# Performance work log

Measured on AMD Instinct MI355X. Metric: run time of the kernel, lower is better.

Reference implementation:

```python
import jax, jax.numpy as jnp
import numpy as np

NEG_SLOPE = 0.2

def symlog(v):
    return jnp.sign(v) * jnp.log1p(jnp.abs(v))

def conv1d(v, w, b):
    # v: (N, Cin, L), w: (Cout, Cin, 3), 'same' padding, stride 1
    out = jax.lax.conv_general_dilated(v, w, (1,), 'SAME',
                                       dimension_numbers=('NCH', 'OIH', 'NCH'))
    return out + b[None, :, None]

def glorot(key, shape, fan_in, fan_out):
    s = jnp.sqrt(6.0 / (fan_in + fan_out))
    return jax.random.uniform(key, shape, jnp.float32, -s, s)

def setup_inputs() -> dict:
    N, L, E = 20000, 128, 320000
    IN, H, C, OHC = 512, 8, 32, 8
    key = jax.random.key(0)
    ks = jax.random.split(key, 12)
    x = jax.random.normal(ks[0], (N, IN), jnp.float32)
    onehot = jax.random.uniform(ks[1], (N, L), jnp.float32)
    src = jax.random.randint(ks[2], (E,), 0, N)
    off = jax.random.randint(ks[3], (E,), 1, N)
    dst = (src + off) % N  # guarantees no self loops
    adj = jnp.stack([src, dst], axis=0).astype(jnp.int64)
    lin_w = glorot(ks[4], (IN + OHC, H * C), IN + OHC, H * C)
    att_l = glorot(ks[5], (1, H, C), C, C)
    att_r = glorot(ks[6], (1, H, C), C, C)
    bias = jnp.zeros((H * C,), jnp.float32)
    conv1_w = glorot(ks[7], (8, 1, 3), 3, 24)
    conv1_b = jnp.zeros((8,), jnp.float32)
    conv2_w = glorot(ks[8], (16, 8, 3), 24, 48)
    conv2_b = jnp.zeros((16,), jnp.float32)
    lin2_w = glorot(ks[9], (16, OHC), 16, OHC)
    lin2_b = jnp.zeros((OHC,), jnp.float32)
    return {"x": x, "onehot": onehot, "adj": adj, "n_nodes": N,
            "lin_w": lin_w, "att_l": att_l, "att_r": att_r, "bias": bias,
            "conv1_w": conv1_w, "conv1_b": conv1_b,
            "conv2_w": conv2_w, "conv2_b": conv2_b,
            "lin2_w": lin2_w, "lin2_b": lin2_b}

def reference(x, onehot, adj, n_nodes, lin_w, att_l, att_r, bias,
              conv1_w, conv1_b, conv2_w, conv2_b, lin2_w, lin2_b):
    N = n_nodes
    H, C = att_l.shape[1], att_l.shape[2]
    # one-hot conv pipe: sort -> symlog -> conv-relu x2 -> global avg pool -> linear
    prepared = symlog(jnp.sort(onehot, axis=-1))[:, None, :]  # (N,1,L)
    h = jax.nn.relu(conv1d(prepared, conv1_w, conv1_b))
    h = jax.nn.relu(conv1d(h, conv2_w, conv2_b))
    readout = h.mean(axis=-1) @ lin2_w + lin2_b  # (N, OHC)
    xin = jnp.concatenate([x, readout], axis=-1)
    xh = (xin @ lin_w).reshape(N, H, C)
    al = (xh * att_l).sum(axis=-1)  # (N,H) sending alphas
    ar = (xh * att_r).sum(axis=-1)  # (N,H) receiving alphas
    # add self loops (input adj has none, so remove_self_loops is a no-op)
    loops = jnp.arange(N, dtype=adj.dtype)
    src = jnp.concatenate([adj[0], loops])
    dst = jnp.concatenate([adj[1], loops])
    # GAT-style attention with segment softmax over receiving nodes
    alpha = jax.nn.leaky_relu(al[src] + ar[dst], NEG_SLOPE)  # (Etot,H)
    amax = jax.ops.segment_max(alpha, dst, num_segments=N)
    ex = jnp.exp(alpha - amax[dst])
    denom = jax.ops.segment_sum(ex, dst, num_segments=N)
    alpha = ex / denom[dst]
    # weight + scatter-add aggregate
    wx = xh[src] * alpha[..., None]  # (Etot,H,C)
    new_x = jax.ops.segment_sum(wx, dst, num_segments=N).reshape(N, H * C) + bias
    new_onehot = jax.ops.segment_sum(onehot[src], dst, num_segments=N) + onehot
    return new_x, new_onehot
```

## Files before the change

### kernel.cpp

```cpp
#include <hip/hip_runtime.h>

#define NEG_SLOPE 0.2f

typedef __attribute__((ext_vector_type(4))) float f32x4;
typedef __attribute__((ext_vector_type(2))) float f32x2;
typedef __attribute__((ext_vector_type(8))) short short8;

__device__ __forceinline__ f32x2 mk2(float a, float b) { f32x2 r; r[0] = a; r[1] = b; return r; }

__device__ __forceinline__ f32x2 FMA2(f32x2 a, f32x2 b, f32x2 c) {
#if __has_builtin(__builtin_elementwise_fma)
    return __builtin_elementwise_fma(a, b, c);
#else
    f32x2 r; r[0] = fmaf(a[0], b[0], c[0]); r[1] = fmaf(a[1], b[1], c[1]); return r;
#endif
}

__device__ __forceinline__ ushort f2bf(float f) {
    uint u = __float_as_uint(f);
    u += 0x7FFFu + ((u >> 16) & 1u);
    return (ushort)(u >> 16);
}
__device__ __forceinline__ float bflo(uint u) { return __uint_as_float(u << 16); }
__device__ __forceinline__ float bfhi(uint u) { return __uint_as_float(u & 0xffff0000u); }


__global__ __launch_bounds__(256) void k_conv_wave(
    const float* __restrict__ x, const float* __restrict__ onehot,
    const float* __restrict__ c1w, const float* __restrict__ c1b,
    const float* __restrict__ c2w, const float* __restrict__ c2b,
    const float* __restrict__ l2w, const float* __restrict__ l2b,
    ushort* __restrict__ xpadA, uint* __restrict__ ohb, int* __restrict__ cursor, int N) {
    __shared__ ushort Hall[4][1056];

    const int gid = blockIdx.x * 256 + threadIdx.x;
    if (gid < N) cursor[gid] = 0;

    const int wave = threadIdx.x >> 6;
    const int lane = threadIdx.x & 63;
    const int n = blockIdx.x * 4 + wave;
    if (n >= N) return;
    ushort* H = Hall[wave];

    const int nt = n >> 6, g16 = (n >> 4) & 3, r16 = n & 15;
    const size_t qstep = ((size_t)nt*17)*4 + g16;

    {
        const float* xp = &x[(size_t)n*512 + lane*8];
        float4 lo = *reinterpret_cast<const float4*>(xp);
        float4 hi = *reinterpret_cast<const float4*>(xp + 4);
        uint4 w;
        w.x = (uint)f2bf(lo.x) | ((uint)f2bf(lo.y) << 16);
        w.y = (uint)f2bf(lo.z) | ((uint)f2bf(lo.w) << 16);
        w.z = (uint)f2bf(hi.x) | ((uint)f2bf(hi.y) << 16);
        w.w = (uint)f2bf(hi.z) | ((uint)f2bf(hi.w) << 16);
        const size_t a = (qstep + (size_t)(lane >> 2)*4)*512 + ((lane & 3)*16 + r16)*8;
        *reinterpret_cast<uint4*>(&xpadA[a]) = w;
    }

    float2 in2 = *reinterpret_cast<const float2*>(&onehot[(size_t)n * 128 + lane * 2]);
    ohb[(size_t)n*64 + lane] = (uint)f2bf(in2.x) | ((uint)f2bf(in2.y) << 16);
    float v0 = log1pf(in2.x);
    float v1 = log1pf(in2.y);

    #pragma unroll
    for (int k = 2; k <= 128; k <<= 1) {
        const bool asc = ((lane & (k >> 1)) == 0);
        #pragma unroll
        for (int j = k >> 1; j >= 2; j >>= 1) {
            const int m = j >> 1;
            float p0 = __shfl_xor(v0, m, 64);
            float p1 = __shfl_xor(v1, m, 64);
            const bool keepmin = (((lane & m) == 0) == asc);
            v0 = keepmin ? fminf(v0, p0) : fmaxf(v0, p0);
            v1 = keepmin ? fminf(v1, p1) : fmaxf(v1, p1);
        }
        float lo = fminf(v0, v1), hi = fmaxf(v0, v1);
        v0 = asc ? lo : hi;
        v1 = asc ? hi : lo;
    }

    float pm = __shfl_up(v1, 1, 64); if (lane == 0)  pm = 0.f;
    float pp = __shfl_down(v0, 1, 64); if (lane == 63) pp = 0.f;

    float h0[8], h1[8];
    {
        const f32x2 xm = mk2(pm, v0), x0 = mk2(v0, v1), xp2 = mk2(v1, pp);
        #pragma unroll
        for (int c = 0; c < 8; ++c) {
            const float w0 = c1w[c*3+0], w1 = c1w[c*3+1], w2 = c1w[c*3+2], b = c1b[c];
            f32x2 h = FMA2(xm, mk2(w0, w0), FMA2(x0, mk2(w1, w1), FMA2(xp2, mk2(w2, w2), mk2(b, b))));
            h0[c] = fmaxf(h[0], 0.f);
            h1[c] = fmaxf(h[1], 0.f);
        }
    }

    {
        if (lane == 0) {
            const uint4 z = make_uint4(0,0,0,0);
            *reinterpret_cast<uint4*>(&H[0*8])   = z;
            *reinterpret_cast<uint4*>(&H[130*8]) = z;
            *reinterpret_cast<uint4*>(&H[65*8])  = z;
        }
        uint4 w0, w1;
        w0.x = (uint)f2bf(h0[0]) | ((uint)f2bf(h0[1]) << 16);
        w0.y = (uint)f2bf(h0[2]) | ((uint)f2bf(h0[3]) << 16);
        w0.z = (uint)f2bf(h0[4]) | ((uint)f2bf(h0[5]) << 16);
        w0.w = (uint)f2bf(h0[6]) | ((uint)f2bf(h0[7]) << 16);
        w1.x = (uint)f2bf(h1[0]) | ((uint)f2bf(h1[1]) << 16);
        w1.y = (uint)f2bf(h1[2]) | ((uint)f2bf(h1[3]) << 16);
        w1.z = (uint)f2bf(h1[4]) | ((uint)f2bf(h1[5]) << 16);
        w1.w = (uint)f2bf(h1[6]) | ((uint)f2bf(h1[7]) << 16);
        *reinterpret_cast<uint4*>(&H[(66 + lane)*8]) = w0;
        *reinterpret_cast<uint4*>(&H[(lane + 1)*8])  = w1;
    }

    const int co = lane & 15;
    const int g2 = lane >> 4;
    short8 bfrag;
    #pragma unroll
    for (int j = 0; j < 8; ++j) bfrag[j] = 0;
    if (g2 < 3) {
        #pragma unroll
        for (int j = 0; j < 8; ++j) bfrag[j] = (short)f2bf(c2w[(co*8 + j)*3 + g2]);
    }
    const float bias_c = c2b[co];
    const f32x4 zacc = (f32x4)0.f;

    float poolv = 0.f;
    #pragma unroll
    for (int s = 0; s < 8; ++s) {
        const int qq = s*16 + co + g2;
        const int slot = (qq >> 1) + (qq & 1)*66;
        short8 afrag = *reinterpret_cast<const short8*>(&H[slot*8]);
        f32x4 d = __builtin_amdgcn_mfma_f32_16x16x32_bf16(afrag, bfrag, zacc, 0, 0, 0);
        poolv += fmaxf(d[0] + bias_c, 0.f);
        poolv += fmaxf(d[1] + bias_c, 0.f);
        poolv += fmaxf(d[2] + bias_c, 0.f);
        poolv += fmaxf(d[3] + bias_c, 0.f);
    }
    poolv += __shfl_xor(poolv, 16, 64);
    poolv += __shfl_xor(poolv, 32, 64);

    float rout = (lane < 8) ? l2b[lane] : 0.f;
    #pragma unroll
    for (int c = 0; c < 16; ++c) {
        float pc = __shfl(poolv, c, 64);
        if (lane < 8) rout = fmaf(pc * (1.f/128.f), l2w[c*8 + lane], rout);
    }
    {
        const size_t qb = (qstep + 16u*4u)*512;
        if (lane < 4) {
            const int i0 = 2*lane, i1 = 2*lane + 1;
            float lo = __shfl(rout, i0, 64);
            float hi = __shfl(rout, i1, 64);
            uint w = (uint)f2bf(lo) | ((uint)f2bf(hi) << 16);
            *reinterpret_cast<uint*>(&xpadA[qb + r16*8 + lane*2]) = w;
        } else if (lane < 7) {
            const int kc = lane - 3;
            const uint4 z = make_uint4(0,0,0,0);
            *reinterpret_cast<uint4*>(&xpadA[qb + (kc*16 + r16)*8]) = z;
        }
    }
}

__global__ __launch_bounds__(256) void k_prep(
    const float* __restrict__ lin_w, ushort* __restrict__ BtT,
    const int* __restrict__ dst, int* __restrict__ cursor, int E) {
    const int gid = blockIdx.x * 256 + threadIdx.x;
    if (gid < E) atomicAdd(&cursor[dst[gid]], 1);
    const int col = blockIdx.x;
    if (col < 256) {
        const int cs = col >> 4, fcol = col & 15;
        for (int k = threadIdx.x; k < 544; k += 256) {
            float v = (k < 520) ? lin_w[(size_t)k*256 + col] : 0.f;
            const int s = k >> 5, kc = (k >> 3) & 3, j = k & 7;
            BtT[(size_t)(s*16 + cs)*512 + (kc*16 + fcol)*8 + j] = f2bf(v);
        }
    }
}

__global__ __launch_bounds__(1024) void k_scan(int* __restrict__ deg, int* __restrict__ row_start, int N) {
    __shared__ int wsum[16];
    const int t = threadIdx.x;
    const int w = t >> 6, ln = t & 63;
    const int base = t * 20;
    int v[20];
    int run = 0;
    #pragma unroll
    for (int i = 0; i < 20; ++i) {
        const int idx = base + i;
        int d = 0;
        if (idx < N) { d = deg[idx]; deg[idx] = 0; }
        run += d;
        v[i] = run;
    }
    int s = run;
    #pragma unroll
    for (int d = 1; d < 64; d <<= 1) {
        int u = __shfl_up(s, d, 64);
        if (ln >= d) s += u;
    }
    if (ln == 63) wsum[w] = s;
    __syncthreads();
    if (w == 0) {
        int ws = (ln < 16) ? wsum[ln] : 0;
        int e2 = ws;
        #pragma unroll
        for (int d = 1; d < 16; d <<= 1) {
            int u = __shfl_up(e2, d, 64);
            if (ln >= d) e2 += u;
        }
        if (ln < 16) wsum[ln] = e2 - ws;
    }
    __syncthreads();
    const int off = (s - run) + wsum[w];
    if (t == 0) row_start[0] = 0;
    #pragma unroll
    for (int i = 0; i < 20; ++i) {
        const int idx = base + i;
        if (idx < N) row_start[idx + 1] = off + v[i];
    }
}

__global__ __launch_bounds__(128) void k_gemm_mfma(
    const ushort* __restrict__ xpadA, const ushort* __restrict__ BtT,
    const float* __restrict__ att_l, const float* __restrict__ att_r,
    ushort* __restrict__ xhb, float* __restrict__ al, float* __restrict__ ar,
    const int* __restrict__ src, const int* __restrict__ dst,
    const int* __restrict__ row_start, int* __restrict__ cursor, int* __restrict__ csr,
    int N, int E) {
    __shared__ __align__(16) float ep[64*36];

    const int t = threadIdx.x;
    const int wv = t >> 6, lane = t & 63;

    const int nwg = gridDim.x;
    const int q = nwg >> 3, r = nwg & 7;
    const int xcd = blockIdx.x & 7, idx = blockIdx.x >> 3;
    const int logical = (xcd < r ? xcd*(q+1) : r*(q+1) + (xcd-r)*q) + idx;
    const int lt = logical >> 3;
    const int ch = logical & 7;
    const int m0 = lt * 64;
    const int c0 = ch * 32;
    const int cs = ch * 2;

    const ushort* A0 = xpadA + ((size_t)(lt*17)*4 + wv*2)*512 + lane*8;
    const ushort* A1 = A0 + 512;
    const ushort* B0 = BtT + (size_t)(cs + 0)*512 + lane*8;
    const ushort* B1 = BtT + (size_t)(cs + 1)*512 + lane*8;

    f32x4 acc00 = (f32x4)0.f, acc01 = (f32x4)0.f, acc10 = (f32x4)0.f, acc11 = (f32x4)0.f;

    short8 a0[4], a1[4], b0[4], b1[4];
#define LOADSET(B_, S_)                                                       \
    {                                                                         \
        a0[B_] = *reinterpret_cast<const short8*>(A0 + (size_t)(S_)*2048);    \
        a1[B_] = *reinterpret_cast<const short8*>(A1 + (size_t)(S_)*2048);    \
        b0[B_] = *reinterpret_cast<const short8*>(B0 + (size_t)(S_)*8192);    \
        b1[B_] = *reinterpret_cast<const short8*>(B1 + (size_t)(S_)*8192);    \
    }
    LOADSET(0, 0)
    LOADSET(1, 1)
    LOADSET(2, 2)
    #pragma unroll
    for (int s = 0; s < 17; ++s) {
        const int b = s & 3;
        if (s + 3 < 17) LOADSET((s + 3) & 3, s + 3)
        acc00 = __builtin_amdgcn_mfma_f32_16x16x32_bf16(a0[b], b0[b], acc00, 0, 0, 0);
        acc01 = __builtin_amdgcn_mfma_f32_16x16x32_bf16(a0[b], b1[b], acc01, 0, 0, 0);
        acc10 = __builtin_amdgcn_mfma_f32_16x16x32_bf16(a1[b], b0[b], acc10, 0, 0, 0);
        acc11 = __builtin_amdgcn_mfma_f32_16x16x32_bf16(a1[b], b1[b], acc11, 0, 0, 0);
    }
#undef LOADSET

    {
        const int e = blockIdx.x * 128 + t;
        if (e < E) {
            const int d = dst[e];
            const int p = atomicAdd(&cursor[d], 1);
            csr[row_start[d] + p] = src[e];
        }
    }

    {
        const int rq = (lane >> 4) * 4;
        const int cb = lane & 15;
        #pragma unroll
        for (int r2 = 0; r2 < 4; ++r2) {
            ep[(wv*32 +      rq + r2)*36 +      cb] = acc00[r2];
            ep[(wv*32 +      rq + r2)*36 + 16 + cb] = acc01[r2];
            ep[(wv*32 + 16 + rq + r2)*36 +      cb] = acc10[r2];
            ep[(wv*32 + 16 + rq + r2)*36 + 16 + cb] = acc11[r2];
        }
    }
    __syncthreads();
    {
        const int rl = t >> 1;
        const int half = t & 1;
        const int row = m0 + rl;
        if (row < N) {
            const float* sp = &ep[rl*36 + half*16];
            float vals[16];
            #pragma unroll
            for (int i = 0; i < 16; ++i) vals[i] = sp[i];
            uint u[8];
            #pragma unroll
            for (int i = 0; i < 8; ++i)
                u[i] = (uint)f2bf(vals[2*i]) | ((uint)f2bf(vals[2*i+1]) << 16);
            ushort* db = &xhb[(size_t)row*256 + c0 + half*16];
            *reinterpret_cast<uint4*>(db)     = make_uint4(u[0], u[1], u[2], u[3]);
            *reinterpret_cast<uint4*>(db + 8) = make_uint4(u[4], u[5], u[6], u[7]);
            float pl = 0.f, pr = 0.f;
            #pragma unroll
            for (int i = 0; i < 16; ++i) {
                pl = fmaf(vals[i], att_l[c0 + half*16 + i], pl);
                pr = fmaf(vals[i], att_r[c0 + half*16 + i], pr);
            }
            pl += __shfl_xor(pl, 1, 64);
            pr += __shfl_xor(pr, 1, 64);
            if (half == 0) {
                al[(size_t)row*8 + ch] = pl;
                ar[(size_t)row*8 + ch] = pr;
            }
        }
    }
}

__global__ __launch_bounds__(256) void k_agg(
    const ushort* __restrict__ xhb,
    const float* __restrict__ al, const float* __restrict__ ar,
    const float* __restrict__ onehot, const uint* __restrict__ ohb,
    const float* __restrict__ bias,
    const int* __restrict__ row_start, const int* __restrict__ csr,
    float* __restrict__ out_x, float* __restrict__ out_oh, int N) {
    const int wave = threadIdx.x >> 6;
    const int lane = threadIdx.x & 63;
    const int half = lane >> 5;
    const int ln = lane & 31;
    const int n = blockIdx.x * 8 + wave * 2 + half;
    if (n >= N) return;
    const int h = ln >> 2;
    const float ard = ar[(size_t)n*8 + h];

    float a_self = al[(size_t)n*8 + h] + ard;
    a_self = fmaxf(a_self, NEG_SLOPE * a_self);
    float e_self = __expf(a_self);
    uint4 xsb = *reinterpret_cast<const uint4*>(&xhb[(size_t)n*256 + ln*8]);
    float acc0 = e_self * bflo(xsb.x), acc1 = e_self * bfhi(xsb.x);
    float acc2 = e_self * bflo(xsb.y), acc3 = e_self * bfhi(xsb.y);
    float acc4 = e_self * bflo(xsb.z), acc5 = e_self * bfhi(xsb.z);
    float acc6 = e_self * bflo(xsb.w), acc7 = e_self * bfhi(xsb.w);
    float den = e_self;
    float oh0 = 0.f, oh1 = 0.f, oh2 = 0.f, oh3 = 0.f;

    const int beg = row_start[n], end = row_start[n+1];
    int i = beg;
    for (; i + 1 < end; i += 2) {
        const int s0 = csr[i], s1 = csr[i+1];
        const float al0 = al[(size_t)s0*8 + h], al1 = al[(size_t)s1*8 + h];
        const uint4 x0 = *reinterpret_cast<const uint4*>(&xhb[(size_t)s0*256 + ln*8]);
        const uint4 x1 = *reinterpret_cast<const uint4*>(&xhb[(size_t)s1*256 + ln*8]);
        const uint2 o0 = *reinterpret_cast<const uint2*>(&ohb[(size_t)s0*64 + ln*2]);
        const uint2 o1 = *reinterpret_cast<const uint2*>(&ohb[(size_t)s1*64 + ln*2]);
        float a0 = al0 + ard; a0 = fmaxf(a0, NEG_SLOPE * a0);
        float a1 = al1 + ard; a1 = fmaxf(a1, NEG_SLOPE * a1);
        const float e0 = __expf(a0), e1 = __expf(a1);
        acc0 = fmaf(e0, bflo(x0.x), fmaf(e1, bflo(x1.x), acc0));
        acc1 = fmaf(e0, bfhi(x0.x), fmaf(e1, bfhi(x1.x), acc1));
        acc2 = fmaf(e0, bflo(x0.y), fmaf(e1, bflo(x1.y), acc2));
        acc3 = fmaf(e0, bfhi(x0.y), fmaf(e1, bfhi(x1.y), acc3));
        acc4 = fmaf(e0, bflo(x0.z), fmaf(e1, bflo(x1.z), acc4));
        acc5 = fmaf(e0, bfhi(x0.z), fmaf(e1, bfhi(x1.z), acc5));
        acc6 = fmaf(e0, bflo(x0.w), fmaf(e1, bflo(x1.w), acc6));
        acc7 = fmaf(e0, bfhi(x0.w), fmaf(e1, bfhi(x1.w), acc7));
        den += e0 + e1;
        oh0 += bflo(o0.x) + bflo(o1.x);
        oh1 += bfhi(o0.x) + bfhi(o1.x);
        oh2 += bflo(o0.y) + bflo(o1.y);
        oh3 += bfhi(o0.y) + bfhi(o1.y);
    }
    if (i < end) {
        const int s0 = csr[i];
        float a0 = al[(size_t)s0*8 + h] + ard;
        a0 = fmaxf(a0, NEG_SLOPE * a0);
        const float e0 = __expf(a0);
        const uint4 x0 = *reinterpret_cast<const uint4*>(&xhb[(size_t)s0*256 + ln*8]);
        const uint2 o0 = *reinterpret_cast<const uint2*>(&ohb[(size_t)s0*64 + ln*2]);
        acc0 = fmaf(e0, bflo(x0.x), acc0);
        acc1 = fmaf(e0, bfhi(x0.x), acc1);
        acc2 = fmaf(e0, bflo(x0.y), acc2);
        acc3 = fmaf(e0, bfhi(x0.y), acc3);
        acc4 = fmaf(e0, bflo(x0.z), acc4);
        acc5 = fmaf(e0, bfhi(x0.z), acc5);
        acc6 = fmaf(e0, bflo(x0.w), acc6);
        acc7 = fmaf(e0, bfhi(x0.w), acc7);
        den += e0;
        oh0 += bflo(o0.x);
        oh1 += bfhi(o0.x);
        oh2 += bflo(o0.y);
        oh3 += bfhi(o0.y);
    }
    const float inv = 1.f / den;
    const float4 bv0 = *reinterpret_cast<const float4*>(&bias[ln*8]);
    const float4 bv1 = *reinterpret_cast<const float4*>(&bias[ln*8 + 4]);
    float4 q0, q1;
    q0.x = fmaf(acc0, inv, bv0.x); q0.y = fmaf(acc1, inv, bv0.y);
    q0.z = fmaf(acc2, inv, bv0.z); q0.w = fmaf(acc3, inv, bv0.w);
    q1.x = fmaf(acc4, inv, bv1.x); q1.y = fmaf(acc5, inv, bv1.y);
    q1.z = fmaf(acc6, inv, bv1.z); q1.w = fmaf(acc7, inv, bv1.w);
    *reinterpret_cast<float4*>(&out_x[(size_t)n*256 + ln*8])     = q0;
    *reinterpret_cast<float4*>(&out_x[(size_t)n*256 + ln*8 + 4]) = q1;
    const float4 so = *reinterpret_cast<const float4*>(&onehot[(size_t)n*128 + ln*4]);
    float4 oo;
    oo.x = oh0 + 2.f*so.x;
    oo.y = oh1 + 2.f*so.y;
    oo.z = oh2 + 2.f*so.z;
    oo.w = oh3 + 2.f*so.w;
    *reinterpret_cast<float4*>(&out_oh[(size_t)n*128 + ln*4]) = oo;
}

extern "C" void kernel_launch(void* const* d_in, const int* in_sizes, int n_in,
                              void* d_out, int out_size, void* d_ws, size_t ws_size,
                              hipStream_t stream) {
    const float* x      = (const float*)d_in[0];
    const float* onehot = (const float*)d_in[1];
    const int*   adj    = (const int*)d_in[2];
    const float* lin_w  = (const float*)d_in[4];
    const float* att_l  = (const float*)d_in[5];
    const float* att_r  = (const float*)d_in[6];
    const float* bias   = (const float*)d_in[7];
    const float* c1w    = (const float*)d_in[8];
    const float* c1b    = (const float*)d_in[9];
    const float* c2w    = (const float*)d_in[10];
    const float* c2b    = (const float*)d_in[11];
    const float* l2w    = (const float*)d_in[12];
    const float* l2b    = (const float*)d_in[13];

    const int N = in_sizes[0] / 512;
    const int E = in_sizes[2] / 2;
    const int* src = adj;
    const int* dst = adj + E;

    float* out_x  = (float*)d_out;
    float* out_oh = out_x + (size_t)N * 256;

    const int NT = (N + 63) / 64;

    ushort* xpadA    = (ushort*)d_ws;
    ushort* BtT      = xpadA + (size_t)NT * 17 * 2048;
    ushort* xhb      = BtT + (size_t)17 * 8192;
    uint*   ohb      = (uint*)(xhb + (size_t)N * 256);
    float*  al       = (float*)(ohb + (size_t)N * 64);
    float*  ar       = al + (size_t)N * 8;
    int*   row_start = (int*)(ar + (size_t)N * 8);
    int*   cursor    = row_start + (N + 1);
    int*   csr       = cursor + N;

    const int EB = (E + 255) / 256;
    const int GB = NT * 8;

    k_conv_wave<<<(N + 3) / 4, 256, 0, stream>>>(x, onehot, c1w, c1b, c2w, c2b, l2w, l2b, xpadA, ohb, cursor, N);
    k_prep<<<EB, 256, 0, stream>>>(lin_w, BtT, dst, cursor, E);
    k_scan<<<1, 1024, 0, stream>>>(cursor, row_start, N);
    k_gemm_mfma<<<GB, 128, 0, stream>>>(xpadA, BtT, att_l, att_r, xhb, al, ar,
                                        src, dst, row_start, cursor, csr, N, E);
    k_agg<<<(N + 7) / 8, 256, 0, stream>>>(xhb, al, ar, onehot, ohb, bias, row_start, csr, out_x, out_oh, N);
}
```

Measured before the change: 163.5 us.

## Halve GEMM row tile and fold degree counting into conv kernel

The MFMA GEMM now computes 32-row tiles, with one 16-row MFMA strip per wave instead of two. This doubles the number of workgroups and adds an occupancy hint in the launch bounds. The epilogue is reworked so four threads share each row, with an extra shuffle step for the attention dot products. Destination-degree counting moves from the prep kernel into the conv kernel, and the cursor array is zeroed with a memset beforehand. The lin_w reformatting becomes its own small 256-block kernel. The aim is better GPU fill and less time spent in the serial prep launch, at the cost of more redundant B-tile loads per output row.

```diff
diff --git a/kernel.cpp b/kernel.cpp
--- a/kernel.cpp
+++ b/kernel.cpp
@@ -30,11 +30,12 @@
     const float* __restrict__ c1w, const float* __restrict__ c1b,
     const float* __restrict__ c2w, const float* __restrict__ c2b,
     const float* __restrict__ l2w, const float* __restrict__ l2b,
-    ushort* __restrict__ xpadA, uint* __restrict__ ohb, int* __restrict__ cursor, int N) {
+    ushort* __restrict__ xpadA, uint* __restrict__ ohb,
+    const int* __restrict__ dstv, int* __restrict__ cursor, int N, int E) {
     __shared__ ushort Hall[4][1056];
 
     const int gid = blockIdx.x * 256 + threadIdx.x;
-    if (gid < N) cursor[gid] = 0;
+    if (gid < E) atomicAdd(&cursor[dstv[gid]], 1);
 
     const int wave = threadIdx.x >> 6;
     const int lane = threadIdx.x & 63;
@@ -164,19 +165,14 @@
     }
 }
 
-__global__ __launch_bounds__(256) void k_prep(
-    const float* __restrict__ lin_w, ushort* __restrict__ BtT,
-    const int* __restrict__ dst, int* __restrict__ cursor, int E) {
-    const int gid = blockIdx.x * 256 + threadIdx.x;
-    if (gid < E) atomicAdd(&cursor[dst[gid]], 1);
+__global__ __launch_bounds__(256) void k_prepB(
+    const float* __restrict__ lin_w, ushort* __restrict__ BtT) {
     const int col = blockIdx.x;
-    if (col < 256) {
-        const int cs = col >> 4, fcol = col & 15;
-        for (int k = threadIdx.x; k < 544; k += 256) {
-            float v = (k < 520) ? lin_w[(size_t)k*256 + col] : 0.f;
-            const int s = k >> 5, kc = (k >> 3) & 3, j = k & 7;
-            BtT[(size_t)(s*16 + cs)*512 + (kc*16 + fcol)*8 + j] = f2bf(v);
-        }
+    const int cs = col >> 4, fcol = col & 15;
+    for (int k = threadIdx.x; k < 544; k += 256) {
+        float v = (k < 520) ? lin_w[(size_t)k*256 + col] : 0.f;
+        const int s = k >> 5, kc = (k >> 3) & 3, j = k & 7;
+        BtT[(size_t)(s*16 + cs)*512 + (kc*16 + fcol)*8 + j] = f2bf(v);
     }
 }
 
@@ -223,14 +219,14 @@
     }
 }
 
-__global__ __launch_bounds__(128) void k_gemm_mfma(
+__global__ __launch_bounds__(128, 6) void k_gemm_mfma(
     const ushort* __restrict__ xpadA, const ushort* __restrict__ BtT,
     const float* __restrict__ att_l, const float* __restrict__ att_r,
     ushort* __restrict__ xhb, float* __restrict__ al, float* __restrict__ ar,
-    const int* __restrict__ src, const int* __restrict__ dst,
+    const int* __restrict__ src, const int* __restrict__ dstv,
     const int* __restrict__ row_start, int* __restrict__ cursor, int* __restrict__ csr,
     int N, int E) {
-    __shared__ __align__(16) float ep[64*36];
+    __shared__ __align__(16) float ep[32*36];
 
     const int t = threadIdx.x;
     const int wv = t >> 6, lane = t & 63;
@@ -241,22 +237,23 @@
     const int logical = (xcd < r ? xcd*(q+1) : r*(q+1) + (xcd-r)*q) + idx;
     const int lt = logical >> 3;
     const int ch = logical & 7;
-    const int m0 = lt * 64;
+    const int m0 = lt * 32;
     const int c0 = ch * 32;
     const int cs = ch * 2;
 
-    const ushort* A0 = xpadA + ((size_t)(lt*17)*4 + wv*2)*512 + lane*8;
-    const ushort* A1 = A0 + 512;
+    const int nt = lt >> 1;
+    const int gbase = (lt & 1) * 2 + wv;
+
+    const ushort* A0 = xpadA + ((size_t)(nt*17)*4 + gbase)*512 + lane*8;
     const ushort* B0 = BtT + (size_t)(cs + 0)*512 + lane*8;
     const ushort* B1 = BtT + (size_t)(cs + 1)*512 + lane*8;
 
-    f32x4 acc00 = (f32x4)0.f, acc01 = (f32x4)0.f, acc10 = (f32x4)0.f, acc11 = (f32x4)0.f;
-
-    short8 a0[4], a1[4], b0[4], b1[4];
+    f32x4 acc0 = (f32x4)0.f, acc1 = (f32x4)0.f;
+
+    short8 a[4], b0[4], b1[4];
 #define LOADSET(B_, S_)                                                       \
     {                                                                         \
-        a0[B_] = *reinterpret_cast<const short8*>(A0 + (size_t)(S_)*2048);    \
-        a1[B_] = *reinterpret_cast<const short8*>(A1 + (size_t)(S_)*2048);    \
+        a[B_]  = *reinterpret_cast<const short8*>(A0 + (size_t)(S_)*2048);    \
         b0[B_] = *reinterpret_cast<const short8*>(B0 + (size_t)(S_)*8192);    \
         b1[B_] = *reinterpret_cast<const short8*>(B1 + (size_t)(S_)*8192);    \
     }
@@ -267,17 +264,15 @@
     for (int s = 0; s < 17; ++s) {
         const int b = s & 3;
         if (s + 3 < 17) LOADSET((s + 3) & 3, s + 3)
-        acc00 = __builtin_amdgcn_mfma_f32_16x16x32_bf16(a0[b], b0[b], acc00, 0, 0, 0);
-        acc01 = __builtin_amdgcn_mfma_f32_16x16x32_bf16(a0[b], b1[b], acc01, 0, 0, 0);
-        acc10 = __builtin_amdgcn_mfma_f32_16x16x32_bf16(a1[b], b0[b], acc10, 0, 0, 0);
-        acc11 = __builtin_amdgcn_mfma_f32_16x16x32_bf16(a1[b], b1[b], acc11, 0, 0, 0);
+        acc0 = __builtin_amdgcn_mfma_f32_16x16x32_bf16(a[b], b0[b], acc0, 0, 0, 0);
+        acc1 = __builtin_amdgcn_mfma_f32_16x16x32_bf16(a[b], b1[b], acc1, 0, 0, 0);
     }
 #undef LOADSET
 
     {
         const int e = blockIdx.x * 128 + t;
         if (e < E) {
-            const int d = dst[e];
+            const int d = dstv[e];
             const int p = atomicAdd(&cursor[d], 1);
             csr[row_start[d] + p] = src[e];
         }
@@ -288,38 +283,36 @@
         const int cb = lane & 15;
         #pragma unroll
         for (int r2 = 0; r2 < 4; ++r2) {
-            ep[(wv*32 +      rq + r2)*36 +      cb] = acc00[r2];
-            ep[(wv*32 +      rq + r2)*36 + 16 + cb] = acc01[r2];
-            ep[(wv*32 + 16 + rq + r2)*36 +      cb] = acc10[r2];
-            ep[(wv*32 + 16 + rq + r2)*36 + 16 + cb] = acc11[r2];
+            ep[(wv*16 + rq + r2)*36 +      cb] = acc0[r2];
+            ep[(wv*16 + rq + r2)*36 + 16 + cb] = acc1[r2];
         }
     }
     __syncthreads();
     {
-        const int rl = t >> 1;
-        const int half = t & 1;
+        const int rl = t >> 2;
+        const int cq = (t & 3) * 8;
         const int row = m0 + rl;
         if (row < N) {
-            const float* sp = &ep[rl*36 + half*16];
-            float vals[16];
+            const float* sp = &ep[rl*36 + cq];
+            float vals[8];
             #pragma unroll
-            for (int i = 0; i < 16; ++i) vals[i] = sp[i];
-            uint u[8];
+            for (int i = 0; i < 8; ++i) vals[i] = sp[i];
+            uint u[4];
             #pragma unroll
-            for (int i = 0; i < 8; ++i)
+            for (int i = 0; i < 4; ++i)
                 u[i] = (uint)f2bf(vals[2*i]) | ((uint)f2bf(vals[2*i+1]) << 16);
-            ushort* db = &xhb[(size_t)row*256 + c0 + half*16];
-            *reinterpret_cast<uint4*>(db)     = make_uint4(u[0], u[1], u[2], u[3]);
-            *reinterpret_cast<uint4*>(db + 8) = make_uint4(u[4], u[5], u[6], u[7]);
+            *reinterpret_cast<uint4*>(&xhb[(size_t)row*256 + c0 + cq]) = make_uint4(u[0], u[1], u[2], u[3]);
             float pl = 0.f, pr = 0.f;
             #pragma unroll
-            for (int i = 0; i < 16; ++i) {
-                pl = fmaf(vals[i], att_l[c0 + half*16 + i], pl);
-                pr = fmaf(vals[i], att_r[c0 + half*16 + i], pr);
+            for (int i = 0; i < 8; ++i) {
+                pl = fmaf(vals[i], att_l[c0 + cq + i], pl);
+                pr = fmaf(vals[i], att_r[c0 + cq + i], pr);
             }
             pl += __shfl_xor(pl, 1, 64);
             pr += __shfl_xor(pr, 1, 64);
-            if (half == 0) {
+            pl += __shfl_xor(pl, 2, 64);
+            pr += __shfl_xor(pr, 2, 64);
+            if ((t & 3) == 0) {
                 al[(size_t)row*8 + ch] = pl;
                 ar[(size_t)row*8 + ch] = pr;
             }
@@ -457,11 +450,12 @@
     int*   cursor    = row_start + (N + 1);
     int*   csr       = cursor + N;
 
-    const int EB = (E + 255) / 256;
-    const int GB = NT * 8;
-
-    k_conv_wave<<<(N + 3) / 4, 256, 0, stream>>>(x, onehot, c1w, c1b, c2w, c2b, l2w, l2b, xpadA, ohb, cursor, N);
-    k_prep<<<EB, 256, 0, stream>>>(lin_w, BtT, dst, cursor, E);
+    const int NT32 = (N + 31) / 32;
+    const int GB = NT32 * 8;
+
+    hipMemsetAsync(cursor, 0, (size_t)N * sizeof(int), stream);
+    k_conv_wave<<<(N + 3) / 4, 256, 0, stream>>>(x, onehot, c1w, c1b, c2w, c2b, l2w, l2b, xpadA, ohb, dst, cursor, N, E);
+    k_prepB<<<256, 256, 0, stream>>>(lin_w, BtT);
     k_scan<<<1, 1024, 0, stream>>>(cursor, row_start, N);
     k_gemm_mfma<<<GB, 128, 0, stream>>>(xpadA, BtT, att_l, att_r, xhb, al, ar,
                                         src, dst, row_start, cursor, csr, N, E);
```

Result: slower. 169.2 us (+3.5%).

## Fuse one-hot conv pipeline into GEMM kernel with LDS-staged A tiles

Applied to the files above, without the earlier changes.

Merges the per-node conv/readout kernel into the projection GEMM. Each 512-thread block now builds its 32-row bf16 A tile (x plus readout) directly in shared memory and computes all 256 output columns, so the padded A matrix no longer makes a round trip through global memory. Zeroing of the degree counters moves from the conv kernel to a hipMemsetAsync. In exchange, every block reloads the full B matrix from L2, uses about 52KB of LDS, and runs the conv work serially over four nodes per wave, which may limit occupancy.

```diff
diff --git a/kernel.cpp b/kernel.cpp
--- a/kernel.cpp
+++ b/kernel.cpp
@@ -25,150 +25,11 @@
 __device__ __forceinline__ float bfhi(uint u) { return __uint_as_float(u & 0xffff0000u); }
 
 
-__global__ __launch_bounds__(256) void k_conv_wave(
-    const float* __restrict__ x, const float* __restrict__ onehot,
-    const float* __restrict__ c1w, const float* __restrict__ c1b,
-    const float* __restrict__ c2w, const float* __restrict__ c2b,
-    const float* __restrict__ l2w, const float* __restrict__ l2b,
-    ushort* __restrict__ xpadA, uint* __restrict__ ohb, int* __restrict__ cursor, int N) {
-    __shared__ ushort Hall[4][1056];
-
-    const int gid = blockIdx.x * 256 + threadIdx.x;
-    if (gid < N) cursor[gid] = 0;
-
-    const int wave = threadIdx.x >> 6;
-    const int lane = threadIdx.x & 63;
-    const int n = blockIdx.x * 4 + wave;
-    if (n >= N) return;
-    ushort* H = Hall[wave];
-
-    const int nt = n >> 6, g16 = (n >> 4) & 3, r16 = n & 15;
-    const size_t qstep = ((size_t)nt*17)*4 + g16;
-
-    {
-        const float* xp = &x[(size_t)n*512 + lane*8];
-        float4 lo = *reinterpret_cast<const float4*>(xp);
-        float4 hi = *reinterpret_cast<const float4*>(xp + 4);
-        uint4 w;
-        w.x = (uint)f2bf(lo.x) | ((uint)f2bf(lo.y) << 16);
-        w.y = (uint)f2bf(lo.z) | ((uint)f2bf(lo.w) << 16);
-        w.z = (uint)f2bf(hi.x) | ((uint)f2bf(hi.y) << 16);
-        w.w = (uint)f2bf(hi.z) | ((uint)f2bf(hi.w) << 16);
-        const size_t a = (qstep + (size_t)(lane >> 2)*4)*512 + ((lane & 3)*16 + r16)*8;
-        *reinterpret_cast<uint4*>(&xpadA[a]) = w;
-    }
-
-    float2 in2 = *reinterpret_cast<const float2*>(&onehot[(size_t)n * 128 + lane * 2]);
-    ohb[(size_t)n*64 + lane] = (uint)f2bf(in2.x) | ((uint)f2bf(in2.y) << 16);
-    float v0 = log1pf(in2.x);
-    float v1 = log1pf(in2.y);
-
-    #pragma unroll
-    for (int k = 2; k <= 128; k <<= 1) {
-        const bool asc = ((lane & (k >> 1)) == 0);
-        #pragma unroll
-        for (int j = k >> 1; j >= 2; j >>= 1) {
-            const int m = j >> 1;
-            float p0 = __shfl_xor(v0, m, 64);
-            float p1 = __shfl_xor(v1, m, 64);
-            const bool keepmin = (((lane & m) == 0) == asc);
-            v0 = keepmin ? fminf(v0, p0) : fmaxf(v0, p0);
-            v1 = keepmin ? fminf(v1, p1) : fmaxf(v1, p1);
-        }
-        float lo = fminf(v0, v1), hi = fmaxf(v0, v1);
-        v0 = asc ? lo : hi;
-        v1 = asc ? hi : lo;
-    }
-
-    float pm = __shfl_up(v1, 1, 64); if (lane == 0)  pm = 0.f;
-    float pp = __shfl_down(v0, 1, 64); if (lane == 63) pp = 0.f;
-
-    float h0[8], h1[8];
-    {
-        const f32x2 xm = mk2(pm, v0), x0 = mk2(v0, v1), xp2 = mk2(v1, pp);
-        #pragma unroll
-        for (int c = 0; c < 8; ++c) {
-            const float w0 = c1w[c*3+0], w1 = c1w[c*3+1], w2 = c1w[c*3+2], b = c1b[c];
-            f32x2 h = FMA2(xm, mk2(w0, w0), FMA2(x0, mk2(w1, w1), FMA2(xp2, mk2(w2, w2), mk2(b, b))));
-            h0[c] = fmaxf(h[0], 0.f);
-            h1[c] = fmaxf(h[1], 0.f);
-        }
-    }
-
-    {
-        if (lane == 0) {
-            const uint4 z = make_uint4(0,0,0,0);
-            *reinterpret_cast<uint4*>(&H[0*8])   = z;
-            *reinterpret_cast<uint4*>(&H[130*8]) = z;
-            *reinterpret_cast<uint4*>(&H[65*8])  = z;
-        }
-        uint4 w0, w1;
-        w0.x = (uint)f2bf(h0[0]) | ((uint)f2bf(h0[1]) << 16);
-        w0.y = (uint)f2bf(h0[2]) | ((uint)f2bf(h0[3]) << 16);
-        w0.z = (uint)f2bf(h0[4]) | ((uint)f2bf(h0[5]) << 16);
-        w0.w = (uint)f2bf(h0[6]) | ((uint)f2bf(h0[7]) << 16);
-        w1.x = (uint)f2bf(h1[0]) | ((uint)f2bf(h1[1]) << 16);
-        w1.y = (uint)f2bf(h1[2]) | ((uint)f2bf(h1[3]) << 16);
-        w1.z = (uint)f2bf(h1[4]) | ((uint)f2bf(h1[5]) << 16);
-        w1.w = (uint)f2bf(h1[6]) | ((uint)f2bf(h1[7]) << 16);
-        *reinterpret_cast<uint4*>(&H[(66 + lane)*8]) = w0;
-        *reinterpret_cast<uint4*>(&H[(lane + 1)*8])  = w1;
-    }
-
-    const int co = lane & 15;
-    const int g2 = lane >> 4;
-    short8 bfrag;
-    #pragma unroll
-    for (int j = 0; j < 8; ++j) bfrag[j] = 0;
-    if (g2 < 3) {
-        #pragma unroll
-        for (int j = 0; j < 8; ++j) bfrag[j] = (short)f2bf(c2w[(co*8 + j)*3 + g2]);
-    }
-    const float bias_c = c2b[co];
-    const f32x4 zacc = (f32x4)0.f;
-
-    float poolv = 0.f;
-    #pragma unroll
-    for (int s = 0; s < 8; ++s) {
-        const int qq = s*16 + co + g2;
-        const int slot = (qq >> 1) + (qq & 1)*66;
-        short8 afrag = *reinterpret_cast<const short8*>(&H[slot*8]);
-        f32x4 d = __builtin_amdgcn_mfma_f32_16x16x32_bf16(afrag, bfrag, zacc, 0, 0, 0);
-        poolv += fmaxf(d[0] + bias_c, 0.f);
-        poolv += fmaxf(d[1] + bias_c, 0.f);
-        poolv += fmaxf(d[2] + bias_c, 0.f);
-        poolv += fmaxf(d[3] + bias_c, 0.f);
-    }
-    poolv += __shfl_xor(poolv, 16, 64);
-    poolv += __shfl_xor(poolv, 32, 64);
-
-    float rout = (lane < 8) ? l2b[lane] : 0.f;
-    #pragma unroll
-    for (int c = 0; c < 16; ++c) {
-        float pc = __shfl(poolv, c, 64);
-        if (lane < 8) rout = fmaf(pc * (1.f/128.f), l2w[c*8 + lane], rout);
-    }
-    {
-        const size_t qb = (qstep + 16u*4u)*512;
-        if (lane < 4) {
-            const int i0 = 2*lane, i1 = 2*lane + 1;
-            float lo = __shfl(rout, i0, 64);
-            float hi = __shfl(rout, i1, 64);
-            uint w = (uint)f2bf(lo) | ((uint)f2bf(hi) << 16);
-            *reinterpret_cast<uint*>(&xpadA[qb + r16*8 + lane*2]) = w;
-        } else if (lane < 7) {
-            const int kc = lane - 3;
-            const uint4 z = make_uint4(0,0,0,0);
-            *reinterpret_cast<uint4*>(&xpadA[qb + (kc*16 + r16)*8]) = z;
-        }
-    }
-}
-
 __global__ __launch_bounds__(256) void k_prep(
     const float* __restrict__ lin_w, ushort* __restrict__ BtT,
-    const int* __restrict__ dst, int* __restrict__ cursor, int E) {
+    const int* __restrict__ dstv, int* __restrict__ cursor, int E) {
     const int gid = blockIdx.x * 256 + threadIdx.x;
-    if (gid < E) atomicAdd(&cursor[dst[gid]], 1);
+    if (gid < E) atomicAdd(&cursor[dstv[gid]], 1);
     const int col = blockIdx.x;
     if (col < 256) {
         const int cs = col >> 4, fcol = col & 15;
@@ -223,84 +84,209 @@
     }
 }
 
-__global__ __launch_bounds__(128) void k_gemm_mfma(
-    const ushort* __restrict__ xpadA, const ushort* __restrict__ BtT,
+__global__ __launch_bounds__(512, 4) void k_mega(
+    const float* __restrict__ x, const float* __restrict__ onehot,
+    const float* __restrict__ c1w, const float* __restrict__ c1b,
+    const float* __restrict__ c2w, const float* __restrict__ c2b,
+    const float* __restrict__ l2w, const float* __restrict__ l2b,
+    const ushort* __restrict__ BtT,
     const float* __restrict__ att_l, const float* __restrict__ att_r,
-    ushort* __restrict__ xhb, float* __restrict__ al, float* __restrict__ ar,
-    const int* __restrict__ src, const int* __restrict__ dst,
+    ushort* __restrict__ xhb, uint* __restrict__ ohb,
+    float* __restrict__ al, float* __restrict__ ar,
+    const int* __restrict__ src, const int* __restrict__ dstv,
     const int* __restrict__ row_start, int* __restrict__ cursor, int* __restrict__ csr,
     int N, int E) {
-    __shared__ __align__(16) float ep[64*36];
+    __shared__ __align__(16) unsigned char smem[52256];
 
     const int t = threadIdx.x;
     const int wv = t >> 6, lane = t & 63;
-
-    const int nwg = gridDim.x;
-    const int q = nwg >> 3, r = nwg & 7;
-    const int xcd = blockIdx.x & 7, idx = blockIdx.x >> 3;
-    const int logical = (xcd < r ? xcd*(q+1) : r*(q+1) + (xcd-r)*q) + idx;
-    const int lt = logical >> 3;
-    const int ch = logical & 7;
-    const int m0 = lt * 64;
-    const int c0 = ch * 32;
-    const int cs = ch * 2;
-
-    const ushort* A0 = xpadA + ((size_t)(lt*17)*4 + wv*2)*512 + lane*8;
-    const ushort* A1 = A0 + 512;
-    const ushort* B0 = BtT + (size_t)(cs + 0)*512 + lane*8;
-    const ushort* B1 = BtT + (size_t)(cs + 1)*512 + lane*8;
+    const int m0 = blockIdx.x * 32;
+
+    ushort* H = (ushort*)(smem + 35360 + wv * 2112);
+    if (lane == 0) {
+        const uint4 z = make_uint4(0,0,0,0);
+        *reinterpret_cast<uint4*>(&H[0*8])   = z;
+        *reinterpret_cast<uint4*>(&H[130*8]) = z;
+        *reinterpret_cast<uint4*>(&H[65*8])  = z;
+    }
+
+    for (int it = 0; it < 4; ++it) {
+        const int r = wv * 4 + it;
+        const int n = m0 + r;
+        if (n < N) {
+            const int g = r >> 4, r16 = r & 15;
+
+            {
+                const float* xp = &x[(size_t)n*512 + lane*8];
+                float4 lo = *reinterpret_cast<const float4*>(xp);
+                float4 hi = *reinterpret_cast<const float4*>(xp + 4);
+                uint4 w;
+                w.x = (uint)f2bf(lo.x) | ((uint)f2bf(lo.y) << 16);
+                w.y = (uint)f2bf(lo.z) | ((uint)f2bf(lo.w) << 16);
+                w.z = (uint)f2bf(hi.x) | ((uint)f2bf(hi.y) << 16);
+                w.w = (uint)f2bf(hi.z) | ((uint)f2bf(hi.w) << 16);
+                const int c = (lane >> 2) * 2 + g;
+                *reinterpret_cast<uint4*>(smem + c*1040 + ((lane & 3)*16 + r16)*16) = w;
+            }
+
+            float2 in2 = *reinterpret_cast<const float2*>(&onehot[(size_t)n * 128 + lane * 2]);
+            ohb[(size_t)n*64 + lane] = (uint)f2bf(in2.x) | ((uint)f2bf(in2.y) << 16);
+            float v0 = log1pf(in2.x);
+            float v1 = log1pf(in2.y);
+
+            #pragma unroll
+            for (int k = 2; k <= 128; k <<= 1) {
+                const bool asc = ((lane & (k >> 1)) == 0);
+                #pragma unroll
+                for (int j = k >> 1; j >= 2; j >>= 1) {
+                    const int m = j >> 1;
+                    float p0 = __shfl_xor(v0, m, 64);
+                    float p1 = __shfl_xor(v1, m, 64);
+                    const bool keepmin = (((lane & m) == 0) == asc);
+                    v0 = keepmin ? fminf(v0, p0) : fmaxf(v0, p0);
+                    v1 = keepmin ? fminf(v1, p1) : fmaxf(v1, p1);
+                }
+                float lo = fminf(v0, v1), hi = fmaxf(v0, v1);
+                v0 = asc ? lo : hi;
+                v1 = asc ? hi : lo;
+            }
+
+            float pm = __shfl_up(v1, 1, 64); if (lane == 0)  pm = 0.f;
+            float pp = __shfl_down(v0, 1, 64); if (lane == 63) pp = 0.f;
+
+            float h0[8], h1[8];
+            {
+                const f32x2 xm = mk2(pm, v0), x0 = mk2(v0, v1), xp2 = mk2(v1, pp);
+                #pragma unroll
+                for (int c = 0; c < 8; ++c) {
+                    const float w0 = c1w[c*3+0], w1 = c1w[c*3+1], w2 = c1w[c*3+2], b = c1b[c];
+                    f32x2 h = FMA2(xm, mk2(w0, w0), FMA2(x0, mk2(w1, w1), FMA2(xp2, mk2(w2, w2), mk2(b, b))));
+                    h0[c] = fmaxf(h[0], 0.f);
+                    h1[c] = fmaxf(h[1], 0.f);
+                }
+            }
+
+            {
+                uint4 w0, w1;
+                w0.x = (uint)f2bf(h0[0]) | ((uint)f2bf(h0[1]) << 16);
+                w0.y = (uint)f2bf(h0[2]) | ((uint)f2bf(h0[3]) << 16);
+                w0.z = (uint)f2bf(h0[4]) | ((uint)f2bf(h0[5]) << 16);
+                w0.w = (uint)f2bf(h0[6]) | ((uint)f2bf(h0[7]) << 16);
+                w1.x = (uint)f2bf(h1[0]) | ((uint)f2bf(h1[1]) << 16);
+                w1.y = (uint)f2bf(h1[2]) | ((uint)f2bf(h1[3]) << 16);
+                w1.z = (uint)f2bf(h1[4]) | ((uint)f2bf(h1[5]) << 16);
+                w1.w = (uint)f2bf(h1[6]) | ((uint)f2bf(h1[7]) << 16);
+                *reinterpret_cast<uint4*>(&H[(66 + lane)*8]) = w0;
+                *reinterpret_cast<uint4*>(&H[(lane + 1)*8])  = w1;
+            }
+
+            const int co = lane & 15;
+            const int g2 = lane >> 4;
+            short8 bfrag;
+            #pragma unroll
+            for (int j = 0; j < 8; ++j) bfrag[j] = 0;
+            if (g2 < 3) {
+                #pragma unroll
+                for (int j = 0; j < 8; ++j) bfrag[j] = (short)f2bf(c2w[(co*8 + j)*3 + g2]);
+            }
+            const float bias_c = c2b[co];
+            const f32x4 zacc = (f32x4)0.f;
+
+            float poolv = 0.f;
+            #pragma unroll
+            for (int s = 0; s < 8; ++s) {
+                const int qq = s*16 + co + g2;
+                const int slot = (qq >> 1) + (qq & 1)*66;
+                short8 afrag = *reinterpret_cast<const short8*>(&H[slot*8]);
+                f32x4 d = __builtin_amdgcn_mfma_f32_16x16x32_bf16(afrag, bfrag, zacc, 0, 0, 0);
+                poolv += fmaxf(d[0] + bias_c, 0.f);
+                poolv += fmaxf(d[1] + bias_c, 0.f);
+                poolv += fmaxf(d[2] + bias_c, 0.f);
+                poolv += fmaxf(d[3] + bias_c, 0.f);
+            }
+            poolv += __shfl_xor(poolv, 16, 64);
+            poolv += __shfl_xor(poolv, 32, 64);
+
+            float rout = (lane < 8) ? l2b[lane] : 0.f;
+            #pragma unroll
+            for (int c = 0; c < 16; ++c) {
+                float pc = __shfl(poolv, c, 64);
+                if (lane < 8) rout = fmaf(pc * (1.f/128.f), l2w[c*8 + lane], rout);
+            }
+            {
+                unsigned char* cb = smem + (32 + g)*1040;
+                if (lane < 4) {
+                    float lo = __shfl(rout, 2*lane, 64);
+                    float hi = __shfl(rout, 2*lane + 1, 64);
+                    uint w = (uint)f2bf(lo) | ((uint)f2bf(hi) << 16);
+                    *reinterpret_cast<uint*>(cb + r16*16 + lane*4) = w;
+                } else if (lane < 7) {
+                    const int kc = lane - 3;
+                    const uint4 z = make_uint4(0,0,0,0);
+                    *reinterpret_cast<uint4*>(cb + (kc*16 + r16)*16) = z;
+                }
+            }
+        }
+    }
+    __syncthreads();
+
+    const int ch = wv;
+    const ushort* B0p = BtT + (size_t)(2*ch)*512 + lane*8;
+    const ushort* B1p = BtT + (size_t)(2*ch + 1)*512 + lane*8;
 
     f32x4 acc00 = (f32x4)0.f, acc01 = (f32x4)0.f, acc10 = (f32x4)0.f, acc11 = (f32x4)0.f;
 
-    short8 a0[4], a1[4], b0[4], b1[4];
-#define LOADSET(B_, S_)                                                       \
-    {                                                                         \
-        a0[B_] = *reinterpret_cast<const short8*>(A0 + (size_t)(S_)*2048);    \
-        a1[B_] = *reinterpret_cast<const short8*>(A1 + (size_t)(S_)*2048);    \
-        b0[B_] = *reinterpret_cast<const short8*>(B0 + (size_t)(S_)*8192);    \
-        b1[B_] = *reinterpret_cast<const short8*>(B1 + (size_t)(S_)*8192);    \
-    }
-    LOADSET(0, 0)
-    LOADSET(1, 1)
-    LOADSET(2, 2)
+    short8 b0b[2], b1b[2];
+#define LOADB(B_, S_)                                                          \
+    {                                                                          \
+        b0b[B_] = *reinterpret_cast<const short8*>(B0p + (size_t)(S_)*8192);   \
+        b1b[B_] = *reinterpret_cast<const short8*>(B1p + (size_t)(S_)*8192);   \
+    }
+    LOADB(0, 0)
     #pragma unroll
     for (int s = 0; s < 17; ++s) {
-        const int b = s & 3;
-        if (s + 3 < 17) LOADSET((s + 3) & 3, s + 3)
-        acc00 = __builtin_amdgcn_mfma_f32_16x16x32_bf16(a0[b], b0[b], acc00, 0, 0, 0);
-        acc01 = __builtin_amdgcn_mfma_f32_16x16x32_bf16(a0[b], b1[b], acc01, 0, 0, 0);
-        acc10 = __builtin_amdgcn_mfma_f32_16x16x32_bf16(a1[b], b0[b], acc10, 0, 0, 0);
-        acc11 = __builtin_amdgcn_mfma_f32_16x16x32_bf16(a1[b], b1[b], acc11, 0, 0, 0);
-    }
-#undef LOADSET
+        const int b = s & 1;
+        if (s + 1 < 17) LOADB((s + 1) & 1, s + 1)
+        short8 a0 = *reinterpret_cast<const short8*>(smem + (s*2 + 0)*1040 + lane*16);
+        short8 a1 = *reinterpret_cast<const short8*>(smem + (s*2 + 1)*1040 + lane*16);
+        acc00 = __builtin_amdgcn_mfma_f32_16x16x32_bf16(a0, b0b[b], acc00, 0, 0, 0);
+        acc01 = __builtin_amdgcn_mfma_f32_16x16x32_bf16(a0, b1b[b], acc01, 0, 0, 0);
+        acc10 = __builtin_amdgcn_mfma_f32_16x16x32_bf16(a1, b0b[b], acc10, 0, 0, 0);
+        acc11 = __builtin_amdgcn_mfma_f32_16x16x32_bf16(a1, b1b[b], acc11, 0, 0, 0);
+    }
+#undef LOADB
 
     {
-        const int e = blockIdx.x * 128 + t;
+        const int e = blockIdx.x * 512 + t;
         if (e < E) {
-            const int d = dst[e];
+            const int d = dstv[e];
             const int p = atomicAdd(&cursor[d], 1);
             csr[row_start[d] + p] = src[e];
         }
     }
+    __syncthreads();
 
     {
+        float* ep = (float*)smem;
         const int rq = (lane >> 4) * 4;
         const int cb = lane & 15;
+        const int c0 = ch * 32;
         #pragma unroll
         for (int r2 = 0; r2 < 4; ++r2) {
-            ep[(wv*32 +      rq + r2)*36 +      cb] = acc00[r2];
-            ep[(wv*32 +      rq + r2)*36 + 16 + cb] = acc01[r2];
-            ep[(wv*32 + 16 + rq + r2)*36 +      cb] = acc10[r2];
-            ep[(wv*32 + 16 + rq + r2)*36 + 16 + cb] = acc11[r2];
+            ep[(     rq + r2)*260 + c0 +      cb] = acc00[r2];
+            ep[(     rq + r2)*260 + c0 + 16 + cb] = acc01[r2];
+            ep[(16 + rq + r2)*260 + c0 +      cb] = acc10[r2];
+            ep[(16 + rq + r2)*260 + c0 + 16 + cb] = acc11[r2];
         }
     }
     __syncthreads();
     {
-        const int rl = t >> 1;
-        const int half = t & 1;
+        const float* ep = (const float*)smem;
+        const int rl = t >> 4;
+        const int cq = (t & 15) * 16;
         const int row = m0 + rl;
         if (row < N) {
-            const float* sp = &ep[rl*36 + half*16];
+            const float* sp = ep + rl*260 + cq;
             float vals[16];
             #pragma unroll
             for (int i = 0; i < 16; ++i) vals[i] = sp[i];
@@ -308,20 +294,21 @@
             #pragma unroll
             for (int i = 0; i < 8; ++i)
                 u[i] = (uint)f2bf(vals[2*i]) | ((uint)f2bf(vals[2*i+1]) << 16);
-            ushort* db = &xhb[(size_t)row*256 + c0 + half*16];
+            ushort* db = &xhb[(size_t)row*256 + cq];
             *reinterpret_cast<uint4*>(db)     = make_uint4(u[0], u[1], u[2], u[3]);
             *reinterpret_cast<uint4*>(db + 8) = make_uint4(u[4], u[5], u[6], u[7]);
             float pl = 0.f, pr = 0.f;
             #pragma unroll
             for (int i = 0; i < 16; ++i) {
-                pl = fmaf(vals[i], att_l[c0 + half*16 + i], pl);
-                pr = fmaf(vals[i], att_r[c0 + half*16 + i], pr);
+                pl = fmaf(vals[i], att_l[cq + i], pl);
+                pr = fmaf(vals[i], att_r[cq + i], pr);
             }
             pl += __shfl_xor(pl, 1, 64);
             pr += __shfl_xor(pr, 1, 64);
-            if (half == 0) {
-                al[(size_t)row*8 + ch] = pl;
-                ar[(size_t)row*8 + ch] = pr;
+            if ((t & 1) == 0) {
+                const int head = (t & 15) >> 1;
+                al[(size_t)row*8 + head] = pl;
+                ar[(size_t)row*8 + head] = pr;
             }
         }
     }
@@ -445,10 +432,7 @@
     float* out_x  = (float*)d_out;
     float* out_oh = out_x + (size_t)N * 256;
 
-    const int NT = (N + 63) / 64;
-
-    ushort* xpadA    = (ushort*)d_ws;
-    ushort* BtT      = xpadA + (size_t)NT * 17 * 2048;
+    ushort* BtT      = (ushort*)d_ws;
     ushort* xhb      = BtT + (size_t)17 * 8192;
     uint*   ohb      = (uint*)(xhb + (size_t)N * 256);
     float*  al       = (float*)(ohb + (size_t)N * 64);
@@ -458,12 +442,13 @@
     int*   csr       = cursor + N;
 
     const int EB = (E + 255) / 256;
-    const int GB = NT * 8;
-
-    k_conv_wave<<<(N + 3) / 4, 256, 0, stream>>>(x, onehot, c1w, c1b, c2w, c2b, l2w, l2b, xpadA, ohb, cursor, N);
+    const int MB = (N + 31) / 32;
+
+    hipMemsetAsync(cursor, 0, (size_t)N * sizeof(int), stream);
     k_prep<<<EB, 256, 0, stream>>>(lin_w, BtT, dst, cursor, E);
     k_scan<<<1, 1024, 0, stream>>>(cursor, row_start, N);
-    k_gemm_mfma<<<GB, 128, 0, stream>>>(xpadA, BtT, att_l, att_r, xhb, al, ar,
-                                        src, dst, row_start, cursor, csr, N, E);
+    k_mega<<<MB, 512, 0, stream>>>(x, onehot, c1w, c1b, c2w, c2b, l2w, l2b,
+                                   BtT, att_l, att_r, xhb, ohb, al, ar,
+                                   src, dst, row_start, cursor, csr, N, E);
     k_agg<<<(N + 7) / 8, 256, 0, stream>>>(xhb, al, ar, onehot, ohb, bias, row_start, csr, out_x, out_oh, N);
 }
```

Measured after the change: 172.6 us. 1.06x slower.
